# Optimization experiments

Measured on AMD Instinct MI355X. Metric: run time of the kernel, lower is better.

The kernel has to match this reference:

```python
import jax, jax.numpy as jnp
import numpy as np


def setup_inputs() -> dict:
    key = jax.random.key(0)
    k1, k2, k3 = jax.random.split(key, 3)
    x = jax.random.normal(k1, (32, 256, 32, 32), dtype=jnp.float32)
    weight = jax.random.normal(k2, (256, 256, 3, 3), dtype=jnp.float32) * 0.05
    bias = jax.random.normal(k3, (256,), dtype=jnp.float32) * 0.01
    return {"x": x, "weight": weight, "bias": bias}


def _forward(x, weight, bias):
    B, cin, n, _ = x.shape
    cout, _, k, _ = weight.shape
    s = (k - 1) // 2
    nf = n // 2 + 1
    bins = n * nf

    # fft shift matrix: exp(-1j*2*pi*s*(i+j)/n), kept rfft columns
    idx = jnp.arange(n)
    shift = idx[None, :] + idx[:, None]                     # (n, n)
    shift_m = jnp.exp(-1j * 2 * jnp.pi * s * shift / n)[:, :nf]
    shift_m = shift_m.reshape(bins, 1, 1).astype(jnp.complex64)

    # xfft: (B, cin, n, nf) -> (bins, cin, B)
    xfft = jnp.fft.rfft2(x)
    xfft = jnp.transpose(xfft, (2, 3, 1, 0)).reshape(bins, cin, B)

    # Hfft: (cout, cin, n, nf) -> (bins, cout, cin), shifted + conj
    Hfft = jnp.fft.rfft2(weight, s=(n, n)).reshape(cout, cin, bins)
    Hfft = shift_m * jnp.conj(jnp.transpose(Hfft, (2, 0, 1)))

    def sq_abs(z):
        return jnp.real(z) ** 2 + jnp.imag(z) ** 2

    RowNorm = jnp.sqrt(jnp.sum(sq_abs(Hfft), axis=2))       # (bins, cout)
    ColNorm = jnp.sqrt(jnp.sum(sq_abs(Hfft), axis=1))       # (bins, cin)

    if cout >= cin:
        RowLoss = jnp.mean((RowNorm - jnp.sqrt(cin / cout)) ** 2)
        ColLoss = jnp.mean((ColNorm - 1.0) ** 2)
        HHT = jnp.einsum('npc,nqc->npq', jnp.conj(Hfft), Hfft)  # (bins, cout, cout)
        mask = jnp.triu(jnp.ones((cout, cout), bool), k=1)
        count = bins * (cout * (cout - 1) // 2)
        AngLoss = jnp.sum(sq_abs(HHT) * mask[None]) / count   # MSE(|HHT[triu]|, 0)
        L = cout * ColLoss + cin * RowLoss + AngLoss
    else:
        RowLoss = jnp.mean((RowNorm - 1.0) ** 2)
        ColLoss = jnp.mean((ColNorm - jnp.sqrt(cout / cin)) ** 2)
        HTH = jnp.einsum('ndp,ndq->npq', jnp.conj(Hfft), Hfft)  # (bins, cin, cin)
        mask = jnp.triu(jnp.ones((cin, cin), bool), k=1)
        count = bins * (cin * (cin - 1) // 2)
        AngLoss = jnp.sum(sq_abs(HTH) * mask[None]) / count
        L = cout * ColLoss + cin * RowLoss + AngLoss

    # per-bin complex matmul: (bins, cout, cin) @ (bins, cin, B) -> (bins, cout, B)
    yfft = Hfft @ xfft
    yfft = jnp.transpose(yfft.reshape(n, nf, cout, B), (3, 2, 0, 1))  # (B, cout, n, nf)
    y = jnp.fft.irfft2(yfft, s=(n, n))
    y = y + bias[None, :, None, None]
    return y, L


def reference(x, weight, bias):
    return _forward(x, weight, bias)
```

## Files before the change

kernel.cpp:

```cpp
#include <hip/hip_runtime.h>
#include <math.h>

typedef __attribute__((ext_vector_type(8)))  short  short8;
typedef __attribute__((ext_vector_type(16))) float  float16;

#define TWO_PI_OVER_32 0.19634954084936207f

static __device__ __forceinline__ unsigned short f2bf(float f) {
    unsigned int u = __float_as_uint(f);
    u = (u + 0x7FFFu + ((u >> 16) & 1u)) >> 16;
    return (unsigned short)u;
}
static __device__ __forceinline__ float bf2f(unsigned short s) {
    return __uint_as_float(((unsigned int)s) << 16);
}

static __device__ __forceinline__ void g2l16(const void* g, void* l) {
    __builtin_amdgcn_global_load_lds(
        (const __attribute__((address_space(1))) unsigned int*)g,
        (__attribute__((address_space(3))) unsigned int*)l, 16, 0, 0);
}

__global__ __launch_bounds__(256) void k_prep(const float* __restrict__ w,
                                              unsigned short* __restrict__ wt,
                                              unsigned short* __restrict__ Vb,
                                              float* __restrict__ Drow,
                                              float* __restrict__ Dcol,
                                              float* __restrict__ accum) {
    __shared__ float sdata[45];
    __shared__ float ws2[256 * 9];
    int blk = blockIdx.x, tid = threadIdx.x, lane = tid & 63;
    bool colmode = blk >= 256;
    int pc = blk & 255;
    if (blk == 0 && tid < 4) accum[tid] = 0.f;
    if (tid < 45) sdata[tid] = 0.f;

    int p = colmode ? tid : pc;
    int c = colmode ? pc : tid;
    float w9[9];
    #pragma unroll
    for (int t = 0; t < 9; ++t) w9[t] = w[(p * 256 + c) * 9 + t];
    if (!colmode) {
        #pragma unroll
        for (int t = 0; t < 9; ++t) ws2[tid * 9 + t] = w9[t];
    }
    __syncthreads();

    int idx = 0;
    for (int ta = 0; ta < 9; ++ta)
        for (int tb = ta; tb < 9; ++tb) {
            float v = w9[ta] * w9[tb];
            #pragma unroll
            for (int off = 32; off > 0; off >>= 1) v += __shfl_down(v, off);
            if (lane == 0) atomicAdd(&sdata[idx], v);
            ++idx;
        }
    __syncthreads();
    if (tid < 45) (colmode ? Dcol : Drow)[pc * 45 + tid] = sdata[tid];

    if (!colmode) {
        #pragma unroll
        for (int t = 0; t < 9; ++t)
            wt[t * 65536 + (c >> 3) * 2048 + p * 8 + (c & 7)] = f2bf(w9[t]);
        if (tid < 320) {
            int ta = tid >> 5, cig = tid & 31;
            union { unsigned short u[8]; uint4 v; } pk;
            #pragma unroll
            for (int u = 0; u < 8; ++u)
                pk.u[u] = (ta < 9) ? f2bf(ws2[(cig * 8 + u) * 9 + ta]) : (unsigned short)0;
            ((uint4*)Vb)[(p * 10 + ta) * 32 + cig] = pk.v;
        }
    }
}

__global__ __launch_bounds__(256) void k_xcvt(const float* __restrict__ x,
                                              unsigned short* __restrict__ xb) {
    int g = blockIdx.x * 256 + threadIdx.x;
    int c = g & 31, r = (g >> 5) & 31, cig = (g >> 10) & 31, b = g >> 15;
    const float* xp = x + ((b * 256 + cig * 8) * 32 + r) * 32 + c;
    union { unsigned short u[8]; uint4 v; } pk;
    #pragma unroll
    for (int u = 0; u < 8; ++u) pk.u[u] = f2bf(xp[u * 1024]);
    ((uint4*)xb)[g] = pk.v;
}

__global__ __launch_bounds__(256, 2) void k_conv(const unsigned short* __restrict__ xb,
                                                 const unsigned short* __restrict__ wt,
                                                 const float* __restrict__ bias,
                                                 float* __restrict__ y) {
    __shared__ unsigned short xs[640 * 8];
    __shared__ unsigned short wsm[1152 * 8];

    const int tid  = threadIdx.x;
    const int lane = tid & 63;
    const int wv   = tid >> 6;
    const int half = lane >> 5;
    const int m    = lane & 31;

    const int id    = blockIdx.x;
    const int xcd   = id & 7;
    const int local = id >> 3;
    const int b     = xcd * 4 + (local >> 4);
    const int rem   = local & 15;
    const int co0   = (rem & 3) * 64;
    const int r0    = (rem >> 2) * 8;

    float16 acc[2][2];
    #pragma unroll
    for (int i = 0; i < 2; ++i)
        #pragma unroll
        for (int ns = 0; ns < 2; ++ns)
            #pragma unroll
            for (int r = 0; r < 16; ++r) acc[i][ns][r] = 0.f;

    const uint4* xbv = (const uint4*)xb;
    const uint4* wtv = (const uint4*)wt;
    uint4* xsv = (uint4*)xs;
    uint4* wsv = (uint4*)wsm;
    const short8* xsl = (const short8*)xs;
    const short8* wsl = (const short8*)wsm;

    const int cigl = lane >> 5;
    const int coll = lane & 31;

    #pragma unroll 1
    for (int kc = 0; kc < 16; ++kc) {
        for (int ch = wv; ch < 10; ch += 4) {
            int gr = (r0 + ch + 31) & 31;
            g2l16(&xbv[((b * 32 + kc * 2 + cigl) * 32 + gr) * 32 + coll],
                  &xsv[ch * 64]);
        }
        for (int ch = wv; ch < 18; ch += 4) {
            int t = ch >> 1, cig = ch & 1;
            g2l16(&wtv[t * 8192 + (kc * 2 + cig) * 256 + co0 + lane],
                  &wsv[ch * 64]);
        }
        __syncthreads();

        #pragma unroll
        for (int t = 0; t < 9; ++t) {
            const int atv = t / 3, btv = t % 3;
            short8 a0 = wsl[(t * 2 + half) * 64 + m];
            short8 a1 = wsl[(t * 2 + half) * 64 + 32 + m];
            #pragma unroll
            for (int ns = 0; ns < 2; ++ns) {
                int slot = wv * 2 + ns + atv;
                short8 bf = xsl[(slot * 2 + half) * 32 + ((m + btv + 31) & 31)];
                acc[0][ns] = __builtin_amdgcn_mfma_f32_32x32x16_bf16(a0, bf, acc[0][ns], 0, 0, 0);
                acc[1][ns] = __builtin_amdgcn_mfma_f32_32x32x16_bf16(a1, bf, acc[1][ns], 0, 0, 0);
            }
        }
        __syncthreads();
    }

    #pragma unroll
    for (int i = 0; i < 2; ++i) {
        #pragma unroll
        for (int ns = 0; ns < 2; ++ns) {
            int r = r0 + wv * 2 + ns;
            #pragma unroll
            for (int reg = 0; reg < 16; ++reg) {
                int crow = (reg & 3) + 8 * (reg >> 2) + 4 * half;
                int co = co0 + i * 32 + crow;
                y[(b * 256 + co) * 1024 + r * 32 + m] = acc[i][ns][reg] + bias[co];
            }
        }
    }
}

__global__ __launch_bounds__(256) void k_rowcol(const float* __restrict__ Drow,
                                                const float* __restrict__ Dcol,
                                                float* __restrict__ accum) {
    int bin = blockIdx.x;
    int u = bin / 17, v = bin % 17;
    __shared__ float coef[45];
    __shared__ float red[2];
    int tid = threadIdx.x;
    if (tid < 2) red[tid] = 0.f;
    if (tid < 45) {
        int idx = 0, TA = 0, TB = 0;
        for (int ta = 0; ta < 9; ++ta)
            for (int tb = ta; tb < 9; ++tb) {
                if (idx == tid) { TA = ta; TB = tb; }
                ++idx;
            }
        int da = TA / 3 - TB / 3;
        int db = TA % 3 - TB % 3;
        float cth = cosf(TWO_PI_OVER_32 * (float)(u * da + v * db));
        coef[tid] = (TA == TB) ? 1.f : 2.f * cth;
    }
    __syncthreads();

    float s1 = 0.f, s2 = 0.f;
    const float* dr = Drow + tid * 45;
    const float* dc = Dcol + tid * 45;
    #pragma unroll
    for (int i = 0; i < 45; ++i) {
        s1 += coef[i] * dr[i];
        s2 += coef[i] * dc[i];
    }
    float e1 = sqrtf(fmaxf(s1, 0.f)) - 1.f; e1 *= e1;
    float e2 = sqrtf(fmaxf(s2, 0.f)) - 1.f; e2 *= e2;
    #pragma unroll
    for (int off = 32; off > 0; off >>= 1) {
        e1 += __shfl_down(e1, off);
        e2 += __shfl_down(e2, off);
    }
    if ((tid & 63) == 0) { atomicAdd(&red[0], e1); atomicAdd(&red[1], e2); }
    __syncthreads();
    if (tid == 0) { atomicAdd(&accum[0], red[0]); atomicAdd(&accum[1], red[1]); }
}

__global__ __launch_bounds__(256) void k_gram(const unsigned short* __restrict__ Vb,
                                              unsigned short* __restrict__ Gb) {
    int blk = blockIdx.x, I = 0;
    while (blk >= 20 - I) { blk -= 20 - I; ++I; }
    int J = I + blk;

    const int tid  = threadIdx.x;
    const int lane = tid & 63;
    const int wave = tid >> 6;
    const int wm = wave >> 1, wn = wave & 1;
    const int half = lane >> 5;
    const int m = lane & 31;

    const int row0 = I * 128 + wm * 64;
    const int col0 = J * 128 + wn * 64;

    float16 acc[2][2];
    #pragma unroll
    for (int i = 0; i < 2; ++i)
        #pragma unroll
        for (int j = 0; j < 2; ++j)
            #pragma unroll
            for (int r = 0; r < 16; ++r) acc[i][j][r] = 0.f;

    const short8* vb = (const short8*)Vb;
    for (int kc = 0; kc < 16; ++kc) {
        int cig = kc * 2 + half;
        short8 a0 = vb[(row0 + m) * 32 + cig];
        short8 a1 = vb[(row0 + 32 + m) * 32 + cig];
        short8 b0 = vb[(col0 + m) * 32 + cig];
        short8 b1 = vb[(col0 + 32 + m) * 32 + cig];
        acc[0][0] = __builtin_amdgcn_mfma_f32_32x32x16_bf16(a0, b0, acc[0][0], 0, 0, 0);
        acc[0][1] = __builtin_amdgcn_mfma_f32_32x32x16_bf16(a0, b1, acc[0][1], 0, 0, 0);
        acc[1][0] = __builtin_amdgcn_mfma_f32_32x32x16_bf16(a1, b0, acc[1][0], 0, 0, 0);
        acc[1][1] = __builtin_amdgcn_mfma_f32_32x32x16_bf16(a1, b1, acc[1][1], 0, 0, 0);
    }
    #pragma unroll
    for (int i = 0; i < 2; ++i)
        #pragma unroll
        for (int j = 0; j < 2; ++j)
            #pragma unroll
            for (int reg = 0; reg < 16; ++reg) {
                int crow = (reg & 3) + 8 * (reg >> 2) + 4 * half;
                Gb[(row0 + i * 32 + crow) * 2560 + col0 + j * 32 + m] =
                    f2bf(acc[i][j][reg]);
            }
}

__global__ __launch_bounds__(256) void k_angred(const unsigned short* __restrict__ Gb,
                                                float* __restrict__ accum) {
    int p = blockIdx.x;
    __shared__ unsigned short gs[9 * 2560];
    __shared__ float red;
    if (threadIdx.x == 0) red = 0.f;
    uint4* gsv = (uint4*)gs;
    const uint4* gbv = (const uint4*)Gb;
    for (int i = threadIdx.x; i < 2880; i += 256) {
        int rr = i / 320, cc = i - rr * 320;
        gsv[i] = gbv[(p * 10 + rr) * 320 + cc];
    }
    __syncthreads();

    int q = threadIdx.x;
    float S = 0.f;
    if (q > p) {
        float g5[5][5];
        #pragma unroll
        for (int i = 0; i < 5; ++i)
            #pragma unroll
            for (int j = 0; j < 5; ++j) g5[i][j] = 0.f;
        #pragma unroll
        for (int ta = 0; ta < 9; ++ta)
            #pragma unroll
            for (int tb = 0; tb < 9; ++tb) {
                float c = bf2f(gs[ta * 2560 + q * 10 + tb]);
                g5[ta / 3 - tb / 3 + 2][ta % 3 - tb % 3 + 2] += c;
            }
        float ReS[5];
        #pragma unroll
        for (int d = 0; d < 5; ++d) {
            float s = 0.f;
            for (int vv = 0; vv < 17; ++vv)
                s += cosf(TWO_PI_OVER_32 * (float)(vv * d));
            ReS[d] = s;
        }
        #pragma unroll
        for (int da = 0; da < 5; ++da)
            #pragma unroll
            for (int d1 = 0; d1 < 5; ++d1)
                #pragma unroll
                for (int d2 = 0; d2 < 5; ++d2) {
                    int dd = d1 - d2; if (dd < 0) dd = -dd;
                    S += g5[da][d1] * g5[da][d2] * ReS[dd];
                }
        S *= 32.f;
    }
    #pragma unroll
    for (int off = 32; off > 0; off >>= 1) S += __shfl_down(S, off);
    if ((threadIdx.x & 63) == 0) atomicAdd(&red, S);
    __syncthreads();
    if (threadIdx.x == 0) atomicAdd(&accum[2], red);
}

__global__ void k_fin(const float* __restrict__ accum, float* __restrict__ out) {
    if (threadIdx.x == 0 && blockIdx.x == 0) {
        float row = accum[0], col = accum[1], ang = accum[2];
        out[8388608] = row / 544.f + col / 544.f + ang / (544.f * 32640.f);
    }
}

extern "C" void kernel_launch(void* const* d_in, const int* in_sizes, int n_in,
                              void* d_out, int out_size, void* d_ws, size_t ws_size,
                              hipStream_t stream) {
    const float* x    = (const float*)d_in[0];
    const float* w    = (const float*)d_in[1];
    const float* bias = (const float*)d_in[2];
    float* out = (float*)d_out;

    char* ws = (char*)d_ws;
    unsigned short* wt = (unsigned short*)ws;
    unsigned short* xb = (unsigned short*)(ws + 1179648);
    unsigned short* Gb = xb;
    unsigned short* Vb = (unsigned short*)(ws + 17956864);
    float* Drow  = (float*)(ws + 19267584);
    float* Dcol  = (float*)(ws + 19313664);
    float* accum = (float*)(ws + 19359744);

    k_prep  <<<512, 256, 0, stream>>>(w, wt, Vb, Drow, Dcol, accum);
    k_xcvt  <<<4096, 256, 0, stream>>>(x, xb);
    k_conv  <<<512, 256, 0, stream>>>(xb, wt, bias, out);
    k_gram  <<<210, 256, 0, stream>>>(Vb, Gb);
    k_rowcol<<<544, 256, 0, stream>>>(Drow, Dcol, accum);
    k_angred<<<256, 256, 0, stream>>>(Gb, accum);
    k_fin   <<<1, 64, 0, stream>>>(accum, out);
}
```

Baseline: 181.5 us.

## Halve conv block tile, cache shifted input fragments in registers, merge loss kernels

The conv kernel now uses 128-thread blocks, each covering 4 output rows instead of 8, and launches twice as many blocks. Each wave preloads the 12 shifted input fragments into registers once per channel chunk instead of re-reading LDS for every tap, and the two global-to-LDS copy loops are merged into one unrolled loop. The row/column loss and angular loss kernels are fused into one launch that branches on block index and shares a union of LDS buffers. The goals are more blocks for occupancy, less LDS read traffic, and one fewer launch, at the cost of more halo reloading per output row and higher register pressure.

After: 189.8 us. 4.6% more time.

```diff
diff --git a/kernel.cpp b/kernel.cpp
--- a/kernel.cpp
+++ b/kernel.cpp
@@ -84,11 +84,11 @@
     ((uint4*)xb)[g] = pk.v;
 }
 
-__global__ __launch_bounds__(256, 2) void k_conv(const unsigned short* __restrict__ xb,
+__global__ __launch_bounds__(128, 2) void k_conv(const unsigned short* __restrict__ xb,
                                                  const unsigned short* __restrict__ wt,
                                                  const float* __restrict__ bias,
                                                  float* __restrict__ y) {
-    __shared__ unsigned short xs[640 * 8];
+    __shared__ unsigned short xs[384 * 8];
     __shared__ unsigned short wsm[1152 * 8];
 
     const int tid  = threadIdx.x;
@@ -100,10 +100,10 @@
     const int id    = blockIdx.x;
     const int xcd   = id & 7;
     const int local = id >> 3;
-    const int b     = xcd * 4 + (local >> 4);
-    const int rem   = local & 15;
+    const int b     = xcd * 4 + (local >> 5);
+    const int rem   = local & 31;
     const int co0   = (rem & 3) * 64;
-    const int r0    = (rem >> 2) * 8;
+    const int r0    = (rem >> 2) * 4;
 
     float16 acc[2][2];
     #pragma unroll
@@ -125,17 +125,27 @@
 
     #pragma unroll 1
     for (int kc = 0; kc < 16; ++kc) {
-        for (int ch = wv; ch < 10; ch += 4) {
-            int gr = (r0 + ch + 31) & 31;
-            g2l16(&xbv[((b * 32 + kc * 2 + cigl) * 32 + gr) * 32 + coll],
-                  &xsv[ch * 64]);
-        }
-        for (int ch = wv; ch < 18; ch += 4) {
-            int t = ch >> 1, cig = ch & 1;
-            g2l16(&wtv[t * 8192 + (kc * 2 + cig) * 256 + co0 + lane],
-                  &wsv[ch * 64]);
-        }
-        __syncthreads();
+        #pragma unroll
+        for (int ch = wv; ch < 24; ch += 2) {
+            if (ch < 6) {
+                int gr = (r0 + ch + 31) & 31;
+                g2l16(&xbv[((b * 32 + kc * 2 + cigl) * 32 + gr) * 32 + coll],
+                      &xsv[ch * 64]);
+            } else {
+                int wc = ch - 6;
+                int t = wc >> 1, cig = wc & 1;
+                g2l16(&wtv[t * 8192 + (kc * 2 + cig) * 256 + co0 + lane],
+                      &wsv[wc * 64]);
+            }
+        }
+        __syncthreads();
+
+        short8 bfr[4][3];
+        #pragma unroll
+        for (int s = 0; s < 4; ++s)
+            #pragma unroll
+            for (int btv = 0; btv < 3; ++btv)
+                bfr[s][btv] = xsl[((wv * 2 + s) * 2 + half) * 32 + ((m + btv + 31) & 31)];
 
         #pragma unroll
         for (int t = 0; t < 9; ++t) {
@@ -144,10 +154,8 @@
             short8 a1 = wsl[(t * 2 + half) * 64 + 32 + m];
             #pragma unroll
             for (int ns = 0; ns < 2; ++ns) {
-                int slot = wv * 2 + ns + atv;
-                short8 bf = xsl[(slot * 2 + half) * 32 + ((m + btv + 31) & 31)];
-                acc[0][ns] = __builtin_amdgcn_mfma_f32_32x32x16_bf16(a0, bf, acc[0][ns], 0, 0, 0);
-                acc[1][ns] = __builtin_amdgcn_mfma_f32_32x32x16_bf16(a1, bf, acc[1][ns], 0, 0, 0);
+                acc[0][ns] = __builtin_amdgcn_mfma_f32_32x32x16_bf16(a0, bfr[ns + atv][btv], acc[0][ns], 0, 0, 0);
+                acc[1][ns] = __builtin_amdgcn_mfma_f32_32x32x16_bf16(a1, bfr[ns + atv][btv], acc[1][ns], 0, 0, 0);
             }
         }
         __syncthreads();
@@ -166,49 +174,6 @@
             }
         }
     }
-}
-
-__global__ __launch_bounds__(256) void k_rowcol(const float* __restrict__ Drow,
-                                                const float* __restrict__ Dcol,
-                                                float* __restrict__ accum) {
-    int bin = blockIdx.x;
-    int u = bin / 17, v = bin % 17;
-    __shared__ float coef[45];
-    __shared__ float red[2];
-    int tid = threadIdx.x;
-    if (tid < 2) red[tid] = 0.f;
-    if (tid < 45) {
-        int idx = 0, TA = 0, TB = 0;
-        for (int ta = 0; ta < 9; ++ta)
-            for (int tb = ta; tb < 9; ++tb) {
-                if (idx == tid) { TA = ta; TB = tb; }
-                ++idx;
-            }
-        int da = TA / 3 - TB / 3;
-        int db = TA % 3 - TB % 3;
-        float cth = cosf(TWO_PI_OVER_32 * (float)(u * da + v * db));
-        coef[tid] = (TA == TB) ? 1.f : 2.f * cth;
-    }
-    __syncthreads();
-
-    float s1 = 0.f, s2 = 0.f;
-    const float* dr = Drow + tid * 45;
-    const float* dc = Dcol + tid * 45;
-    #pragma unroll
-    for (int i = 0; i < 45; ++i) {
-        s1 += coef[i] * dr[i];
-        s2 += coef[i] * dc[i];
-    }
-    float e1 = sqrtf(fmaxf(s1, 0.f)) - 1.f; e1 *= e1;
-    float e2 = sqrtf(fmaxf(s2, 0.f)) - 1.f; e2 *= e2;
-    #pragma unroll
-    for (int off = 32; off > 0; off >>= 1) {
-        e1 += __shfl_down(e1, off);
-        e2 += __shfl_down(e2, off);
-    }
-    if ((tid & 63) == 0) { atomicAdd(&red[0], e1); atomicAdd(&red[1], e2); }
-    __syncthreads();
-    if (tid == 0) { atomicAdd(&accum[0], red[0]); atomicAdd(&accum[1], red[1]); }
 }
 
 __global__ __launch_bounds__(256) void k_gram(const unsigned short* __restrict__ Vb,
@@ -259,59 +224,103 @@
             }
 }
 
-__global__ __launch_bounds__(256) void k_angred(const unsigned short* __restrict__ Gb,
-                                                float* __restrict__ accum) {
-    int p = blockIdx.x;
-    __shared__ unsigned short gs[9 * 2560];
-    __shared__ float red;
-    if (threadIdx.x == 0) red = 0.f;
-    uint4* gsv = (uint4*)gs;
-    const uint4* gbv = (const uint4*)Gb;
-    for (int i = threadIdx.x; i < 2880; i += 256) {
-        int rr = i / 320, cc = i - rr * 320;
-        gsv[i] = gbv[(p * 10 + rr) * 320 + cc];
-    }
-    __syncthreads();
-
-    int q = threadIdx.x;
-    float S = 0.f;
-    if (q > p) {
-        float g5[5][5];
-        #pragma unroll
-        for (int i = 0; i < 5; ++i)
-            #pragma unroll
-            for (int j = 0; j < 5; ++j) g5[i][j] = 0.f;
-        #pragma unroll
-        for (int ta = 0; ta < 9; ++ta)
-            #pragma unroll
-            for (int tb = 0; tb < 9; ++tb) {
-                float c = bf2f(gs[ta * 2560 + q * 10 + tb]);
-                g5[ta / 3 - tb / 3 + 2][ta % 3 - tb % 3 + 2] += c;
-            }
-        float ReS[5];
-        #pragma unroll
-        for (int d = 0; d < 5; ++d) {
-            float s = 0.f;
-            for (int vv = 0; vv < 17; ++vv)
-                s += cosf(TWO_PI_OVER_32 * (float)(vv * d));
-            ReS[d] = s;
-        }
-        #pragma unroll
-        for (int da = 0; da < 5; ++da)
-            #pragma unroll
-            for (int d1 = 0; d1 < 5; ++d1)
+__global__ __launch_bounds__(256) void k_loss(const float* __restrict__ Drow,
+                                              const float* __restrict__ Dcol,
+                                              const unsigned short* __restrict__ Gb,
+                                              float* __restrict__ accum) {
+    __shared__ union {
+        struct { float coef[45]; float red[2]; } rc;
+        struct { unsigned short gs[9 * 2560]; float red; } ang;
+    } sh;
+    int tid = threadIdx.x;
+
+    if (blockIdx.x < 544) {
+        int bin = blockIdx.x;
+        int u = bin / 17, v = bin % 17;
+        if (tid < 2) sh.rc.red[tid] = 0.f;
+        if (tid < 45) {
+            int idx = 0, TA = 0, TB = 0;
+            for (int ta = 0; ta < 9; ++ta)
+                for (int tb = ta; tb < 9; ++tb) {
+                    if (idx == tid) { TA = ta; TB = tb; }
+                    ++idx;
+                }
+            int da = TA / 3 - TB / 3;
+            int db = TA % 3 - TB % 3;
+            float cth = cosf(TWO_PI_OVER_32 * (float)(u * da + v * db));
+            sh.rc.coef[tid] = (TA == TB) ? 1.f : 2.f * cth;
+        }
+        __syncthreads();
+
+        float s1 = 0.f, s2 = 0.f;
+        const float* dr = Drow + tid * 45;
+        const float* dc = Dcol + tid * 45;
+        #pragma unroll
+        for (int i = 0; i < 45; ++i) {
+            s1 += sh.rc.coef[i] * dr[i];
+            s2 += sh.rc.coef[i] * dc[i];
+        }
+        float e1 = sqrtf(fmaxf(s1, 0.f)) - 1.f; e1 *= e1;
+        float e2 = sqrtf(fmaxf(s2, 0.f)) - 1.f; e2 *= e2;
+        #pragma unroll
+        for (int off = 32; off > 0; off >>= 1) {
+            e1 += __shfl_down(e1, off);
+            e2 += __shfl_down(e2, off);
+        }
+        if ((tid & 63) == 0) { atomicAdd(&sh.rc.red[0], e1); atomicAdd(&sh.rc.red[1], e2); }
+        __syncthreads();
+        if (tid == 0) { atomicAdd(&accum[0], sh.rc.red[0]); atomicAdd(&accum[1], sh.rc.red[1]); }
+    } else {
+        int p = blockIdx.x - 544;
+        if (tid == 0) sh.ang.red = 0.f;
+        uint4* gsv = (uint4*)sh.ang.gs;
+        const uint4* gbv = (const uint4*)Gb;
+        for (int i = tid; i < 2880; i += 256) {
+            int rr = i / 320, cc = i - rr * 320;
+            gsv[i] = gbv[(p * 10 + rr) * 320 + cc];
+        }
+        __syncthreads();
+
+        int q = tid;
+        float S = 0.f;
+        if (q > p) {
+            float g5[5][5];
+            #pragma unroll
+            for (int i = 0; i < 5; ++i)
                 #pragma unroll
-                for (int d2 = 0; d2 < 5; ++d2) {
-                    int dd = d1 - d2; if (dd < 0) dd = -dd;
-                    S += g5[da][d1] * g5[da][d2] * ReS[dd];
+                for (int j = 0; j < 5; ++j) g5[i][j] = 0.f;
+            #pragma unroll
+            for (int ta = 0; ta < 9; ++ta)
+                #pragma unroll
+                for (int tb = 0; tb < 9; ++tb) {
+                    float c = bf2f(sh.ang.gs[ta * 2560 + q * 10 + tb]);
+                    g5[ta / 3 - tb / 3 + 2][ta % 3 - tb % 3 + 2] += c;
                 }
-        S *= 32.f;
-    }
-    #pragma unroll
-    for (int off = 32; off > 0; off >>= 1) S += __shfl_down(S, off);
-    if ((threadIdx.x & 63) == 0) atomicAdd(&red, S);
-    __syncthreads();
-    if (threadIdx.x == 0) atomicAdd(&accum[2], red);
+            float ReS[5];
+            #pragma unroll
+            for (int d = 0; d < 5; ++d) {
+                float s = 0.f;
+                for (int vv = 0; vv < 17; ++vv)
+                    s += cosf(TWO_PI_OVER_32 * (float)(vv * d));
+                ReS[d] = s;
+            }
+            #pragma unroll
+            for (int da = 0; da < 5; ++da)
+                #pragma unroll
+                for (int d1 = 0; d1 < 5; ++d1)
+                    #pragma unroll
+                    for (int d2 = 0; d2 < 5; ++d2) {
+                        int dd = d1 - d2; if (dd < 0) dd = -dd;
+                        S += g5[da][d1] * g5[da][d2] * ReS[dd];
+                    }
+            S *= 32.f;
+        }
+        #pragma unroll
+        for (int off = 32; off > 0; off >>= 1) S += __shfl_down(S, off);
+        if ((tid & 63) == 0) atomicAdd(&sh.ang.red, S);
+        __syncthreads();
+        if (tid == 0) atomicAdd(&accum[2], sh.ang.red);
+    }
 }
 
 __global__ void k_fin(const float* __restrict__ accum, float* __restrict__ out) {
@@ -340,9 +349,8 @@
 
     k_prep  <<<512, 256, 0, stream>>>(w, wt, Vb, Drow, Dcol, accum);
     k_xcvt  <<<4096, 256, 0, stream>>>(x, xb);
-    k_conv  <<<512, 256, 0, stream>>>(xb, wt, bias, out);
+    k_conv  <<<1024, 128, 0, stream>>>(xb, wt, bias, out);
     k_gram  <<<210, 256, 0, stream>>>(Vb, Gb);
-    k_rowcol<<<544, 256, 0, stream>>>(Drow, Dcol, accum);
-    k_angred<<<256, 256, 0, stream>>>(Gb, accum);
+    k_loss  <<<800, 256, 0, stream>>>(Drow, Dcol, Gb, accum);
     k_fin   <<<1, 64, 0, stream>>>(accum, out);
 }
```
